# Kernel optimization log

Measured on AMD Instinct MI355X. Metric: run time of the kernel, lower is better.

The kernel has to match this reference:

```python
import jax, jax.numpy as jnp
import numpy as np
from jax import lax

B, TENC, TBERT, TOUT = 16, 168, 96, 200
NMEL, ENC, ARNN, DRNN, PRE, ATT, NF, K = 80, 512, 1024, 1024, 256, 128, 32, 31
PAD = (K - 1) // 2


def setup_inputs():
    key = jax.random.key(0)
    ks = iter(jax.random.split(key, 40))
    def rn(shape, s=0.05):
        return jax.random.normal(next(ks), shape, dtype=jnp.float32) * s
    return dict(
        memory=rn((B, TENC, ENC), 1.0),
        embeddings=rn((B, TBERT, ENC), 1.0),
        decoder_inputs=rn((B, NMEL, TOUT), 1.0),
        prenet_w1=rn((PRE, NMEL)), prenet_w2=rn((PRE, PRE)),
        prenetb_w1=rn((PRE, NMEL)), prenetb_w2=rn((PRE, PRE)),
        arnn_wih=rn((4 * ARNN, PRE + ENC)), arnn_whh=rn((4 * ARNN, ARNN)), arnn_b=rn((4 * ARNN,)),
        arnnb_wih=rn((4 * ARNN, PRE + ENC)), arnnb_whh=rn((4 * ARNN, ARNN)), arnnb_b=rn((4 * ARNN,)),
        attn_q=rn((ATT, ARNN)), attn_m=rn((ATT, ENC)), attn_conv=rn((NF, 2, K)),
        attn_loc=rn((ATT, NF)), attn_v=rn((ATT,)),
        attnb_q=rn((ATT, ARNN)), attnb_m=rn((ATT, ENC)), attnb_conv=rn((NF, 2, K)),
        attnb_loc=rn((ATT, NF)), attnb_v=rn((ATT,)),
        drnn_wih=rn((4 * DRNN, 2 * ARNN + 2 * ENC)), drnn_whh=rn((4 * DRNN, DRNN)), drnn_b=rn((4 * DRNN,)),
        drnnb_wih=rn((4 * DRNN, ARNN + ENC)), drnnb_whh=rn((4 * DRNN, DRNN)), drnnb_b=rn((4 * DRNN,)),
        proj_w=rn((NMEL, DRNN + 2 * ENC)), proj_b=rn((NMEL,)),
        gate_w=rn((1, DRNN + 2 * ENC)), gate_b=rn((1,)),
    )


def _lstm(x, h, c, wih, whh, b):
    g = x @ wih.T + h @ whh.T + b
    i, f, gg, o = jnp.split(g, 4, axis=-1)
    c = jax.nn.sigmoid(f) * c + jax.nn.sigmoid(i) * jnp.tanh(gg)
    h = jax.nn.sigmoid(o) * jnp.tanh(c)
    return h, c


def _lsa(query, mem, pmem, aw, awc, qW, convW, locW, v):
    # location-sensitive attention (Tacotron2)
    pq = query @ qW.T                                   # [B, ATT]
    cat = jnp.stack([aw, awc], axis=1)                  # [B, 2, T]
    fmap = lax.conv_general_dilated(cat, convW, (1,), [(PAD, PAD)],
                                    dimension_numbers=('NCH', 'OIH', 'NCH'))  # [B, NF, T]
    ploc = jnp.einsum('bft,af->bta', fmap, locW)        # [B, T, ATT]
    e = jnp.einsum('a,bta->bt', v, jnp.tanh(pq[:, None, :] + ploc + pmem))
    w = jax.nn.softmax(e, axis=-1)
    ctx = jnp.einsum('bt,bte->be', w, mem)
    return ctx, w


def _forward(memory, embeddings, decoder_inputs, prenet_w1, prenet_w2, prenetb_w1, prenetb_w2,
             arnn_wih, arnn_whh, arnn_b, arnnb_wih, arnnb_whh, arnnb_b,
             attn_q, attn_m, attn_conv, attn_loc, attn_v,
             attnb_q, attnb_m, attnb_conv, attnb_loc, attnb_v,
             drnn_wih, drnn_whh, drnn_b, drnnb_wih, drnnb_whh, drnnb_b,
             proj_w, proj_b, gate_w, gate_b):
    Bv, Tenc, enc = memory.shape
    Tbert = embeddings.shape[1]
    nmel = decoder_inputs.shape[1]
    arnn = arnn_whh.shape[1]
    drnn = drnn_whh.shape[1]
    pmem = jnp.einsum('bte,ae->bta', memory, attn_m)
    pbert = jnp.einsum('bte,ae->bta', embeddings, attnb_m)
    frames = jnp.moveaxis(decoder_inputs, 2, 0)         # [T, B, nmel]
    go = jnp.zeros((1, Bv, nmel), decoder_inputs.dtype)
    xs = jnp.concatenate([go, frames[:-1]], axis=0)     # teacher forcing (shifted)
    z = lambda d: jnp.zeros((Bv, d), memory.dtype)
    carry0 = (z(arnn), z(arnn), z(arnn), z(arnn), z(drnn), z(drnn), z(drnn), z(drnn),
              jnp.zeros((Bv, Tenc), memory.dtype), jnp.zeros((Bv, Tenc), memory.dtype),
              jnp.zeros((Bv, Tbert), memory.dtype), jnp.zeros((Bv, Tbert), memory.dtype),
              z(enc), z(enc))

    def step(carry, x):
        ah, ac, ahb, acb, dh, dc, dhb, dcb, aw, awc, awb, awcb, ctx, ctxb = carry
        p = jax.nn.relu(jax.nn.relu(x @ prenet_w1.T) @ prenet_w2.T)
        pb = jax.nn.relu(jax.nn.relu(x @ prenetb_w1.T) @ prenetb_w2.T)
        ah, ac = _lstm(jnp.concatenate([p, ctx], -1), ah, ac, arnn_wih, arnn_whh, arnn_b)
        ahb, acb = _lstm(jnp.concatenate([pb, ctxb], -1), ahb, acb, arnnb_wih, arnnb_whh, arnnb_b)
        ctx, aw = _lsa(ah, memory, pmem, aw, awc, attn_q, attn_conv, attn_loc, attn_v)
        awc = awc + aw
        ctxb, awb = _lsa(ahb, embeddings, pbert, awb, awcb, attnb_q, attnb_conv, attnb_loc, attnb_v)
        awcb = awcb + awb
        dh, dc = _lstm(jnp.concatenate([ah, ahb, ctx, ctxb], -1), dh, dc, drnn_wih, drnn_whh, drnn_b)
        dhb, dcb = _lstm(jnp.concatenate([ahb, ctxb], -1), dhb, dcb, drnnb_wih, drnnb_whh, drnnb_b)
        hcat = jnp.concatenate([dh, ctx, ctxb], -1)
        mel = hcat @ proj_w.T + proj_b
        gate = (hcat @ gate_w.T + gate_b)[:, 0]
        new_carry = (ah, ac, ahb, acb, dh, dc, dhb, dcb, aw, awc, awb, awcb, ctx, ctxb)
        return new_carry, (mel, gate, aw, awb)

    _, (mels, gates, aligns, alignsb) = lax.scan(step, carry0, xs)
    mel_out = jnp.transpose(mels, (1, 2, 0))            # [B, nmel, T]
    gate_out = jnp.transpose(gates, (1, 0))             # [B, T]
    align_out = jnp.transpose(aligns, (1, 0, 2))        # [B, T, Tenc]
    alignb_out = jnp.transpose(alignsb, (1, 0, 2))      # [B, T, Tbert]
    return mel_out, gate_out, align_out, alignb_out


def reference(memory, embeddings, decoder_inputs, prenet_w1, prenet_w2, prenetb_w1, prenetb_w2,
              arnn_wih, arnn_whh, arnn_b, arnnb_wih, arnnb_whh, arnnb_b,
              attn_q, attn_m, attn_conv, attn_loc, attn_v,
              attnb_q, attnb_m, attnb_conv, attnb_loc, attnb_v,
              drnn_wih, drnn_whh, drnn_b, drnnb_wih, drnnb_whh, drnnb_b,
              proj_w, proj_b, gate_w, gate_b):
    return _forward(memory, embeddings, decoder_inputs, prenet_w1, prenet_w2, prenetb_w1, prenetb_w2,
                    arnn_wih, arnn_whh, arnn_b, arnnb_wih, arnnb_whh, arnnb_b,
                    attn_q, attn_m, attn_conv, attn_loc, attn_v,
                    attnb_q, attnb_m, attnb_conv, attnb_loc, attnb_v,
                    drnn_wih, drnn_whh, drnn_b, drnnb_wih, drnnb_whh, drnnb_b,
                    proj_w, proj_b, gate_w, gate_b)
```

## Files before the change

kernel.cpp:

```cpp
#include <hip/hip_runtime.h>
#include <cstdint>
#include <cmath>

#define DEVI __device__ __forceinline__

constexpr int B_ = 16, TENC_ = 168, TBERT_ = 96, TOUT_ = 200;
constexpr int NMEL_ = 80, ENC_ = 512, ARNN_ = 1024, PRE_ = 256, ATT_ = 128, NF_ = 32, KCV_ = 31;

constexpr size_t o_qWTa = 0;
constexpr size_t o_qWTb = o_qWTa + 1024*128;
constexpr size_t o_pall  = o_qWTb + 1024*128;
constexpr size_t o_pball = o_pall + (size_t)TOUT_*B_*PRE_;
constexpr size_t o_pmem  = o_pball + (size_t)TOUT_*B_*PRE_;
constexpr size_t o_pbert = o_pmem + (size_t)B_*TENC_*ATT_;
constexpr size_t o_state = o_pbert + (size_t)B_*TBERT_*ATT_;
constexpr size_t o_ah   = o_state;
constexpr size_t o_ahb  = o_ah  + 2*B_*ARNN_;
constexpr size_t o_ac   = o_ahb + 2*B_*ARNN_;
constexpr size_t o_acb  = o_ac  + B_*ARNN_;
constexpr size_t o_dh   = o_acb + B_*ARNN_;
constexpr size_t o_dc   = o_dh  + B_*ARNN_;
constexpr size_t o_dhb  = o_dc  + B_*ARNN_;
constexpr size_t o_dcb  = o_dhb + B_*ARNN_;
constexpr size_t o_ctx  = o_dcb + B_*ARNN_;
constexpr size_t o_ctxb = o_ctx + B_*ENC_;
constexpr size_t o_aw   = o_ctxb+ B_*ENC_;
constexpr size_t o_awc  = o_aw  + B_*TENC_;
constexpr size_t o_awb  = o_awc + B_*TENC_;
constexpr size_t o_awcb = o_awb + B_*TBERT_;
constexpr size_t o_zend = o_awcb+ B_*TBERT_;
constexpr size_t ZCOUNT = o_zend - o_state;
constexpr size_t o_gd   = o_zend;
constexpr size_t o_gdb  = o_gd + 4096*B_;
constexpr size_t o_dhall   = o_gdb + 4096*B_;
constexpr size_t o_ctxall  = o_dhall + (size_t)TOUT_*B_*ARNN_;
constexpr size_t o_ctxball = o_ctxall + (size_t)TOUT_*B_*ENC_;

constexpr size_t OO_MEL  = 0;
constexpr size_t OO_GATE = (size_t)B_*NMEL_*TOUT_;
constexpr size_t OO_AL   = OO_GATE + (size_t)B_*TOUT_;
constexpr size_t OO_ALB  = OO_AL + (size_t)B_*TOUT_*TENC_;

DEVI float sigf(float x) { return 1.f / (1.f + expf(-x)); }

DEVI float dotseg(const float* __restrict__ w, const float* __restrict__ x, int n) {
  const float4* wp = reinterpret_cast<const float4*>(w);
  const float4* xp = reinterpret_cast<const float4*>(x);
  float a0 = 0, a1 = 0, a2 = 0, a3 = 0;
  int n4 = n >> 2;
#pragma unroll 4
  for (int i = 0; i < n4; ++i) {
    float4 wv = wp[i], xv = xp[i];
    a0 = fmaf(wv.x, xv.x, a0); a1 = fmaf(wv.y, xv.y, a1);
    a2 = fmaf(wv.z, xv.z, a2); a3 = fmaf(wv.w, xv.w, a3);
  }
  return (a0 + a1) + (a2 + a3);
}

__global__ __launch_bounds__(256) void k_prolog(
    const float* __restrict__ dec, const float* __restrict__ pw1, const float* __restrict__ pw2,
    const float* __restrict__ pbw1, const float* __restrict__ pbw2,
    const float* __restrict__ memory, const float* __restrict__ embeddings,
    const float* __restrict__ am, const float* __restrict__ abm,
    const float* __restrict__ aq, const float* __restrict__ abq,
    float* __restrict__ ws)
{
  __shared__ float smem[10240];
  int bid = blockIdx.x, tid = threadIdx.x;
  if (bid < 200) {
    int t = bid;
    float* xl  = smem;
    float* h1  = smem + 1280;
    float* h1b = smem + 1280 + 4096;
    for (int i = tid; i < 16*80; i += 256) {
      int b = i / 80, m = i % 80;
      xl[i] = (t == 0) ? 0.f : dec[((size_t)b*80 + m)*200 + (t-1)];
    }
    __syncthreads();
    int j = tid;
    for (int b = 0; b < 16; ++b) {
      const float* x = xl + b*80;
      float a1 = 0, a2 = 0;
#pragma unroll 4
      for (int m = 0; m < 80; ++m) { a1 = fmaf(pw1[j*80+m], x[m], a1); a2 = fmaf(pbw1[j*80+m], x[m], a2); }
      h1[b*256+j]  = fmaxf(a1, 0.f);
      h1b[b*256+j] = fmaxf(a2, 0.f);
    }
    __syncthreads();
    for (int b = 0; b < 16; ++b) {
      float a1 = 0, a2 = 0;
#pragma unroll 4
      for (int k = 0; k < 256; ++k) { a1 = fmaf(pw2[j*256+k], h1[b*256+k], a1); a2 = fmaf(pbw2[j*256+k], h1b[b*256+k], a2); }
      ws[o_pall  + ((size_t)t*16+b)*256 + j] = fmaxf(a1, 0.f);
      ws[o_pball + ((size_t)t*16+b)*256 + j] = fmaxf(a2, 0.f);
    }
  } else if (bid < 368) {
    int r0 = (bid - 200) * 16;
    float* ml = smem;
    for (int i = tid; i < 16*512; i += 256) ml[i] = memory[(size_t)r0*512 + i];
    __syncthreads();
    int a = tid & 127, ro = tid >> 7;
    for (int row = ro; row < 16; row += 2) {
      const float* x = ml + row*512; const float* w = am + (size_t)a*512;
      float acc = 0;
#pragma unroll 4
      for (int e = 0; e < 512; ++e) acc = fmaf(w[e], x[e], acc);
      ws[o_pmem + (size_t)(r0+row)*128 + a] = acc;
    }
  } else if (bid < 464) {
    int r0 = (bid - 368) * 16;
    float* ml = smem;
    for (int i = tid; i < 16*512; i += 256) ml[i] = embeddings[(size_t)r0*512 + i];
    __syncthreads();
    int a = tid & 127, ro = tid >> 7;
    for (int row = ro; row < 16; row += 2) {
      const float* x = ml + row*512; const float* w = abm + (size_t)a*512;
      float acc = 0;
#pragma unroll 4
      for (int e = 0; e < 512; ++e) acc = fmaf(w[e], x[e], acc);
      ws[o_pbert + (size_t)(r0+row)*128 + a] = acc;
    }
  } else if (bid < 466) {
    const float* src = (bid == 464) ? aq : abq;
    float* dst = ws + ((bid == 464) ? o_qWTa : o_qWTb);
    for (int i = tid; i < 1024*128; i += 256) {
      int k = i >> 7, a = i & 127;
      dst[i] = src[(size_t)a*1024 + k];
    }
  } else {
    int zi = bid - 466;
    for (size_t i = (size_t)zi*256 + tid; i < ZCOUNT; i += 8*256) ws[o_state + i] = 0.f;
  }
}


DEVI void compute_group(const float4* __restrict__ xsf, int g, int lane,
                        const float4 w[8], float acc[8][16]) {
#pragma unroll
  for (int b = 0; b < 16; ++b) {
    float4 xv = xsf[b*130 + g*64 + lane];
#pragma unroll
    for (int r = 0; r < 8; ++r) {
      acc[r][b] = fmaf(w[r].x, xv.x, acc[r][b]);
      acc[r][b] = fmaf(w[r].y, xv.y, acc[r][b]);
      acc[r][b] = fmaf(w[r].z, xv.z, acc[r][b]);
      acc[r][b] = fmaf(w[r].w, xv.w, acc[r][b]);
    }
  }
}

template<int IH>
DEVI void lstm_gates(const float* __restrict__ Wih, const float* __restrict__ Whh,
                     const float* const pieces[4], const int plens[4], int np,
                     const float* __restrict__ hp,
                     int u0, int wvi, int lane, int tid, float* __restrict__ smem,
                     float acc[8][16])
{
#pragma unroll 1
  for (int sub = 0; sub < 2; ++sub) {
    const float* W = sub ? Whh : Wih;
    const int len = sub ? 1024 : IH;
#pragma unroll 1
    for (int c0 = 0; c0 < len; c0 += 512) {
      const int n = (len - c0 < 512) ? (len - c0) : 512;
      __syncthreads();
      if (sub == 0) {
#pragma unroll 1
        for (int b = 0; b < 16; ++b)
          for (int k = tid; k < n; k += 256) {
            int off = c0 + k;
            const float* src = pieces[0]; int L = plens[0];
            if (np > 1 && off >= L) {
              off -= L; src = pieces[1]; L = plens[1];
              if (np > 2 && off >= L) {
                off -= L; src = pieces[2]; L = plens[2];
                if (np > 3 && off >= L) { off -= L; src = pieces[3]; L = plens[3]; }
              }
            }
            smem[b*520 + k] = src[(size_t)b*L + off];
          }
      } else {
#pragma unroll 1
        for (int b = 0; b < 16; ++b)
          for (int k = tid; k < n; k += 256)
            smem[b*520 + k] = hp[b*1024 + c0 + k];
      }
      __syncthreads();
      const int ng = n >> 8;
      const float* wbase = W + (size_t)(wvi*1024 + u0)*len + c0 + 4*lane;
      const float4* xsf = (const float4*)smem;
      float4 w0[8], w1[8];
#pragma unroll
      for (int r = 0; r < 8; ++r) w0[r] = *(const float4*)(wbase + (size_t)r*len);
      if (ng == 2) {
#pragma unroll
        for (int r = 0; r < 8; ++r) w1[r] = *(const float4*)(wbase + (size_t)r*len + 256);
        compute_group(xsf, 0, lane, w0, acc);
        compute_group(xsf, 1, lane, w1, acc);
      } else {
        compute_group(xsf, 0, lane, w0, acc);
      }
    }
  }
}

DEVI void wave_reduce(float acc[8][16], float* __restrict__ red, int lane, float res[4]) {
  int o = lane & 31, half = lane >> 5;
#pragma unroll
  for (int ph = 0; ph < 4; ++ph) {
#pragma unroll
    for (int j = 0; j < 32; ++j)
      red[j*68 + lane] = acc[2*ph + (j >> 4)][j & 15];
    float s = 0;
    const float* rrow = red + o*68 + half*32;
#pragma unroll
    for (int j = 0; j < 8; ++j) {
      float4 v = *(const float4*)(rrow + 4*j);
      s += (v.x + v.y) + (v.z + v.w);
    }
    res[ph] = s + __shfl_xor(s, 32);
  }
}

__global__ __launch_bounds__(256, 2) void k_step1(
    int t,
    const float* __restrict__ a_wih, const float* __restrict__ a_whh, const float* __restrict__ a_b,
    const float* __restrict__ ab_wih, const float* __restrict__ ab_whh, const float* __restrict__ ab_b,
    const float* __restrict__ d_wih, const float* __restrict__ d_whh,
    const float* __restrict__ db_wih, const float* __restrict__ db_whh,
    float* __restrict__ ws)
{
  __shared__ __align__(16) float smem[8704];
  __shared__ float gbuf[512];
  int bid = blockIdx.x, tid = threadIdx.x;
  int wvi = tid >> 6, lane = tid & 63;
  int type = bid >> 7, idx = bid & 127, u0 = idx * 8;

  float acc[8][16];
#pragma unroll
  for (int r = 0; r < 8; ++r)
#pragma unroll
    for (int b = 0; b < 16; ++b) acc[r][b] = 0.f;

  float res[4];
  int o = lane & 31;

  if (type <= 1) {
    if (t >= TOUT_) return;
    bool isB = (type == 1);
    const float* pieces[4] = { ws + (isB ? o_pball : o_pall) + (size_t)t*B_*PRE_,
                               ws + (isB ? o_ctxb : o_ctx), nullptr, nullptr };
    const int plens[4] = { 256, 512, 0, 0 };
    const float* hp = ws + (isB ? o_ahb : o_ah) + (size_t)((t+1)&1)*(B_*ARNN_);
    lstm_gates<768>(isB ? ab_wih : a_wih, isB ? ab_whh : a_whh, pieces, plens, 2, hp,
                    u0, wvi, lane, tid, smem, acc);
    __syncthreads();
    wave_reduce(acc, smem + wvi*(32*68), lane, res);
    const float* bias = isB ? ab_b : a_b;
#pragma unroll
    for (int ph = 0; ph < 4; ++ph) {
      if (lane < 32) {
        int j = 2*ph + (o >> 4), b = o & 15;
        gbuf[wvi*128 + j*16 + b] = res[ph] + bias[wvi*1024 + u0 + j];
      }
    }
    __syncthreads();
    if (tid < 128) {
      int j = tid >> 4, b = tid & 15, u = u0 + j;
      float gi = gbuf[0*128 + j*16 + b], gf = gbuf[1*128 + j*16 + b];
      float gg = gbuf[2*128 + j*16 + b], go = gbuf[3*128 + j*16 + b];
      float* cst  = ws + (isB ? o_acb : o_ac);
      float* hcur = ws + (isB ? o_ahb : o_ah) + (size_t)(t&1)*(B_*ARNN_);
      float co = cst[u*16 + b];
      float cn = sigf(gf)*co + sigf(gi)*tanhf(gg);
      float hn = sigf(go)*tanhf(cn);
      cst[u*16 + b] = cn;
      hcur[b*1024 + u] = hn;
    }
  } else if (type == 2) {
    if (t == 0) return;
    const float* pieces[4] = { ws + o_ah  + (size_t)((t-1)&1)*(B_*ARNN_),
                               ws + o_ahb + (size_t)((t-1)&1)*(B_*ARNN_),
                               ws + o_ctx, ws + o_ctxb };
    const int plens[4] = { 1024, 1024, 512, 512 };
    lstm_gates<3072>(d_wih, d_whh, pieces, plens, 4, ws + o_dh,
                     u0, wvi, lane, tid, smem, acc);
    __syncthreads();
    wave_reduce(acc, smem + wvi*(32*68), lane, res);
    float* gout = ws + o_gd;
#pragma unroll
    for (int ph = 0; ph < 4; ++ph)
      if (lane < 32)
        gout[(size_t)(wvi*1024 + u0 + 2*ph + (o >> 4))*16 + (o & 15)] = res[ph];
  } else {
    if (t == 0) return;
    const float* pieces[4] = { ws + o_ahb + (size_t)((t-1)&1)*(B_*ARNN_),
                               ws + o_ctxb, nullptr, nullptr };
    const int plens[4] = { 1024, 512, 0, 0 };
    lstm_gates<1536>(db_wih, db_whh, pieces, plens, 2, ws + o_dhb,
                     u0, wvi, lane, tid, smem, acc);
    __syncthreads();
    wave_reduce(acc, smem + wvi*(32*68), lane, res);
    float* gout = ws + o_gdb;
#pragma unroll
    for (int ph = 0; ph < 4; ++ph)
      if (lane < 32)
        gout[(size_t)(wvi*1024 + u0 + 2*ph + (o >> 4))*16 + (o & 15)] = res[ph];
  }
}

__global__ __launch_bounds__(512) void k_step2(
    int t, const float* __restrict__ memory, const float* __restrict__ embeddings,
    const float* __restrict__ a_conv, const float* __restrict__ a_loc, const float* __restrict__ a_v,
    const float* __restrict__ ab_conv, const float* __restrict__ ab_loc, const float* __restrict__ ab_v,
    const float* __restrict__ d_b, const float* __restrict__ db_b,
    float* __restrict__ ws, float* __restrict__ out)
{
  __shared__ float ah_l[1024];
  __shared__ float pqp[4][128];
  __shared__ float pq_s[128];
  __shared__ float awp[2][TENC_+32];
  __shared__ float cw_s[NF_*2*KCV_];
  __shared__ float vv[128];
  __shared__ float fmT[TENC_][NF_];
  __shared__ float ep[TENC_][2];
  __shared__ float wl[TENC_];
  __shared__ float smx[2];
  int bid = blockIdx.x, tid = threadIdx.x;

  if (bid < 32) {
    if (t >= TOUT_) return;
    bool isB = bid >= 16; int b = bid & 15;
    int T = isB ? TBERT_ : TENC_;
    const float* mem   = isB ? embeddings : memory;
    const float* pmemB = ws + (isB ? o_pbert : o_pmem);
    const float* qWT   = ws + (isB ? o_qWTb : o_qWTa);
    const float* convW = isB ? ab_conv : a_conv;
    const float* locW  = isB ? ab_loc : a_loc;
    const float* vW    = isB ? ab_v : a_v;
    const float* hq = ws + (isB ? o_ahb : o_ah) + (size_t)(t&1)*(B_*ARNN_) + b*ARNN_;
    float* awS  = ws + (isB ? o_awb : o_aw) + b*T;
    float* awcS = ws + (isB ? o_awcb : o_awc) + b*T;
    float* ctxS = ws + (isB ? o_ctxb : o_ctx) + b*ENC_;
    float* ctxAll = ws + (isB ? o_ctxball : o_ctxall) + ((size_t)t*16 + b)*ENC_;
    float* alOut = out + (isB ? OO_ALB : OO_AL) + ((size_t)b*TOUT_ + t)*T;

    for (int i = tid; i < 1024; i += 512) ah_l[i] = hq[i];
    for (int i = tid; i < NF_*2*KCV_; i += 512) cw_s[i] = convW[i];
    for (int i = tid; i < 128; i += 512) vv[i] = vW[i];
    for (int i = tid; i < T + 30; i += 512) {
      bool in = (i >= 15) && (i < T + 15);
      awp[0][i] = in ? awS[i-15] : 0.f;
      awp[1][i] = in ? awcS[i-15] : 0.f;
    }
    __syncthreads();
    {
      int a = tid & 127, hf = tid >> 7;
      float acc = 0;
      for (int k = hf*256; k < hf*256 + 256; ++k) acc = fmaf(qWT[(size_t)k*128 + a], ah_l[k], acc);
      pqp[hf][a] = acc;
    }
    __syncthreads();
    if (tid < 128) pq_s[tid] = pqp[0][tid] + pqp[1][tid] + pqp[2][tid] + pqp[3][tid];
    __syncthreads();
    for (int idx = tid; idx < T*NF_; idx += 512) {
      int tt = idx >> 5, f = idx & 31;
      const float* c0 = cw_s + f*62;
      float s = 0;
#pragma unroll
      for (int kk = 0; kk < 31; ++kk)
        s = fmaf(awp[0][tt+kk], c0[kk], fmaf(awp[1][tt+kk], c0[31+kk], s));
      fmT[tt][f] = s;
    }
    __syncthreads();
    {
      int a = tid & 127;
      float la[32];
#pragma unroll
      for (int f = 0; f < 32; ++f) la[f] = locW[a*32 + f];
      float pqr = pq_s[a], vr = vv[a];
      for (int idx = tid; idx < T*128; idx += 512) {
        int tt = idx >> 7;
        float pl = 0;
#pragma unroll
        for (int f = 0; f < 32; ++f) pl = fmaf(fmT[tt][f], la[f], pl);
        float s = vr * tanhf(pqr + pl + pmemB[((size_t)b*T + tt)*128 + a]);
#pragma unroll
        for (int off = 1; off < 64; off <<= 1) s += __shfl_xor(s, off);
        if ((tid & 63) == 0) ep[tt][(idx >> 6) & 1] = s;
      }
    }
    __syncthreads();
    if (tid < 64) {
      float m = -1e30f;
      for (int i = tid; i < T; i += 64) m = fmaxf(m, ep[i][0] + ep[i][1]);
#pragma unroll
      for (int off = 1; off < 64; off <<= 1) m = fmaxf(m, __shfl_xor(m, off));
      float ssum = 0;
      for (int i = tid; i < T; i += 64) ssum += expf(ep[i][0] + ep[i][1] - m);
#pragma unroll
      for (int off = 1; off < 64; off <<= 1) ssum += __shfl_xor(ssum, off);
      if (tid == 0) { smx[0] = m; smx[1] = 1.f / ssum; }
    }
    __syncthreads();
    for (int i = tid; i < T; i += 512) {
      float wv = expf(ep[i][0] + ep[i][1] - smx[0]) * smx[1];
      wl[i] = wv;
      awS[i] = wv;
      awcS[i] += wv;
      alOut[i] = wv;
    }
    __syncthreads();
    {
      float a0 = 0, a1 = 0, a2 = 0, a3 = 0;
      const float* mb = mem + (size_t)b*T*512 + tid;
      int tt = 0;
      for (; tt + 4 <= T; tt += 4) {
        a0 = fmaf(wl[tt],   mb[(size_t)tt*512],     a0);
        a1 = fmaf(wl[tt+1], mb[(size_t)(tt+1)*512], a1);
        a2 = fmaf(wl[tt+2], mb[(size_t)(tt+2)*512], a2);
        a3 = fmaf(wl[tt+3], mb[(size_t)(tt+3)*512], a3);
      }
      for (; tt < T; ++tt) a0 = fmaf(wl[tt], mb[(size_t)tt*512], a0);
      float acc = (a0 + a1) + (a2 + a3);
      ctxS[tid] = acc;
      ctxAll[tid] = acc;
    }
  } else {
    if (t == 0) return;
    int gid = (bid - 32)*512 + tid;
#pragma unroll
    for (int r = 0; r < 2; ++r) {
      int uf = gid + r*16384;
      int L = uf >> 14;
      int rem = uf & 16383;
      int u = rem >> 4, b = rem & 15;
      const float* g = ws + (L ? o_gdb : o_gd);
      const float* bias = L ? db_b : d_b;
      float* h  = ws + (L ? o_dhb : o_dh);
      float* cc = ws + (L ? o_dcb : o_dc);
      float gi = g[(size_t)u*16 + b]        + bias[u];
      float gf = g[(size_t)(1024+u)*16 + b] + bias[1024+u];
      float gg = g[(size_t)(2048+u)*16 + b] + bias[2048+u];
      float go = g[(size_t)(3072+u)*16 + b] + bias[3072+u];
      float co = cc[u*16 + b];
      float cn = sigf(gf)*co + sigf(gi)*tanhf(gg);
      float hn = sigf(go)*tanhf(cn);
      cc[u*16 + b] = cn;
      h[b*1024 + u] = hn;
      if (L == 0) ws[o_dhall + ((size_t)(t-1)*16 + b)*1024 + u] = hn;
    }
  }
}

__global__ __launch_bounds__(512) void k_proj(
    const float* __restrict__ pw, const float* __restrict__ pb,
    const float* __restrict__ gw, const float* __restrict__ gb,
    const float* __restrict__ ws, float* __restrict__ out)
{
  int t = blockIdx.x, tid = threadIdx.x;
  for (int o = tid; o < 16*81; o += 512) {
    int b = o / 81, j = o % 81;
    const float* wrow = (j < 80) ? (pw + (size_t)j*2048) : gw;
    const float* xd  = ws + o_dhall   + ((size_t)t*16 + b)*1024;
    const float* xc  = ws + o_ctxall  + ((size_t)t*16 + b)*512;
    const float* xcb = ws + o_ctxball + ((size_t)t*16 + b)*512;
    float acc = dotseg(wrow, xd, 1024) + dotseg(wrow + 1024, xc, 512)
              + dotseg(wrow + 1536, xcb, 512) + ((j < 80) ? pb[j] : gb[0]);
    if (j < 80) out[OO_MEL + ((size_t)b*80 + j)*200 + t] = acc;
    else        out[OO_GATE + (size_t)b*200 + t] = acc;
  }
}

extern "C" void kernel_launch(void* const* d_in, const int* in_sizes, int n_in,
                              void* d_out, int out_size, void* d_ws, size_t ws_size,
                              hipStream_t stream) {
  (void)in_sizes; (void)n_in; (void)out_size; (void)ws_size;
  const float* memory   = (const float*)d_in[0];
  const float* embeddings = (const float*)d_in[1];
  const float* dec      = (const float*)d_in[2];
  const float* pw1      = (const float*)d_in[3];
  const float* pw2      = (const float*)d_in[4];
  const float* pbw1     = (const float*)d_in[5];
  const float* pbw2     = (const float*)d_in[6];
  const float* a_wih    = (const float*)d_in[7];
  const float* a_whh    = (const float*)d_in[8];
  const float* a_b      = (const float*)d_in[9];
  const float* ab_wih   = (const float*)d_in[10];
  const float* ab_whh   = (const float*)d_in[11];
  const float* ab_b     = (const float*)d_in[12];
  const float* a_q      = (const float*)d_in[13];
  const float* a_m      = (const float*)d_in[14];
  const float* a_conv   = (const float*)d_in[15];
  const float* a_loc    = (const float*)d_in[16];
  const float* a_v      = (const float*)d_in[17];
  const float* ab_q     = (const float*)d_in[18];
  const float* ab_m     = (const float*)d_in[19];
  const float* ab_conv  = (const float*)d_in[20];
  const float* ab_loc   = (const float*)d_in[21];
  const float* ab_v     = (const float*)d_in[22];
  const float* d_wih    = (const float*)d_in[23];
  const float* d_whh    = (const float*)d_in[24];
  const float* d_b      = (const float*)d_in[25];
  const float* db_wih   = (const float*)d_in[26];
  const float* db_whh   = (const float*)d_in[27];
  const float* db_b     = (const float*)d_in[28];
  const float* proj_w   = (const float*)d_in[29];
  const float* proj_b   = (const float*)d_in[30];
  const float* gate_w   = (const float*)d_in[31];
  const float* gate_b   = (const float*)d_in[32];
  float* ws  = (float*)d_ws;
  float* out = (float*)d_out;

  k_prolog<<<dim3(474), dim3(256), 0, stream>>>(dec, pw1, pw2, pbw1, pbw2,
      memory, embeddings, a_m, ab_m, a_q, ab_q, ws);
  for (int t = 0; t <= TOUT_; ++t) {
    k_step1<<<dim3(512), dim3(256), 0, stream>>>(t,
        a_wih, a_whh, a_b, ab_wih, ab_whh, ab_b, d_wih, d_whh, db_wih, db_whh, ws);
    k_step2<<<dim3(64), dim3(512), 0, stream>>>(t, memory, embeddings,
        a_conv, a_loc, a_v, ab_conv, ab_loc, ab_v, d_b, db_b, ws, out);
  }
  k_proj<<<dim3(200), dim3(512), 0, stream>>>(proj_w, proj_b, gate_w, gate_b, ws, out);
}
```

Baseline: 34.28 ms.

## Fuse per-step kernels into a persistent cooperative kernel with grid syncs

```diff
diff --git a/kernel.cpp b/kernel.cpp
--- a/kernel.cpp
+++ b/kernel.cpp
@@ -1,6 +1,9 @@
 #include <hip/hip_runtime.h>
+#include <hip/hip_cooperative_groups.h>
 #include <cstdint>
 #include <cmath>
+
+namespace cg = cooperative_groups;
 
 #define DEVI __device__ __forceinline__
 
@@ -57,6 +60,12 @@
   return (a0 + a1) + (a2 + a3);
 }
 
+DEVI void gl_lds16(const float* g, float* l) {
+  auto gp = (const __attribute__((address_space(1))) float*)g;
+  auto lp = (__attribute__((address_space(3))) float*)l;
+  __builtin_amdgcn_global_load_lds(gp, lp, 16, 0, 0);
+}
+
 __global__ __launch_bounds__(256) void k_prolog(
     const float* __restrict__ dec, const float* __restrict__ pw1, const float* __restrict__ pw2,
     const float* __restrict__ pbw1, const float* __restrict__ pbw2,
@@ -133,73 +142,59 @@
   }
 }
 
-
-DEVI void compute_group(const float4* __restrict__ xsf, int g, int lane,
-                        const float4 w[8], float acc[8][16]) {
+DEVI const float* seg_src(int type, int k0, int b, int t, const float* __restrict__ ws) {
+  if (type <= 1) {
+    if (k0 < 256)  return ws + (type ? o_pball : o_pall) + ((size_t)t*16 + b)*256 + k0;
+    if (k0 < 768)  return ws + (type ? o_ctxb : o_ctx) + (size_t)b*512 + (k0 - 256);
+    return ws + (type ? o_ahb : o_ah) + (size_t)((t+1)&1)*(B_*ARNN_) + (size_t)b*1024 + (k0 - 768);
+  } else if (type == 2) {
+    int tp = (t-1) & 1;
+    if (k0 < 1024) return ws + o_ah  + (size_t)tp*(B_*ARNN_) + (size_t)b*1024 + k0;
+    if (k0 < 2048) return ws + o_ahb + (size_t)tp*(B_*ARNN_) + (size_t)b*1024 + (k0-1024);
+    if (k0 < 2560) return ws + o_ctx  + (size_t)b*512 + (k0-2048);
+    if (k0 < 3072) return ws + o_ctxb + (size_t)b*512 + (k0-2560);
+    return ws + o_dh + (size_t)b*1024 + (k0-3072);
+  } else {
+    int tp = (t-1) & 1;
+    if (k0 < 1024) return ws + o_ahb + (size_t)tp*(B_*ARNN_) + (size_t)b*1024 + k0;
+    if (k0 < 1536) return ws + o_ctxb + (size_t)b*512 + (k0-1024);
+    return ws + o_dhb + (size_t)b*1024 + (k0-1536);
+  }
+}
+
+DEVI void fillr(int type, int r, float* __restrict__ dst, int wl, int lane, int t,
+                const float* __restrict__ ws) {
+  int k0 = r * 256;
+#pragma unroll
+  for (int o = 0; o < 4; ++o) {
+    int b = o*4 + wl;
+    const float* s = seg_src(type, k0, b, t, ws) + 4*lane;
+    gl_lds16(s, dst + b*256);
+  }
+}
+
+DEVI void loadw(float4 w[8], const float* __restrict__ Wih, const float* __restrict__ Whh,
+                int IH, int row0, int r, int lane) {
+  int k0 = r * 256;
+  const float* base; size_t st;
+  if (k0 < IH) { base = Wih + (size_t)row0*IH + k0; st = IH; }
+  else         { base = Whh + (size_t)row0*1024 + (k0 - IH); st = 1024; }
+  base += 4*lane;
+#pragma unroll
+  for (int i = 0; i < 8; ++i) w[i] = *(const float4*)(base + st*i);
+}
+
+DEVI void computeg(const float* __restrict__ buf, const float4 w[8], int lane, float acc[8][16]) {
+  const float4* xb = (const float4*)buf;
 #pragma unroll
   for (int b = 0; b < 16; ++b) {
-    float4 xv = xsf[b*130 + g*64 + lane];
-#pragma unroll
-    for (int r = 0; r < 8; ++r) {
-      acc[r][b] = fmaf(w[r].x, xv.x, acc[r][b]);
-      acc[r][b] = fmaf(w[r].y, xv.y, acc[r][b]);
-      acc[r][b] = fmaf(w[r].z, xv.z, acc[r][b]);
-      acc[r][b] = fmaf(w[r].w, xv.w, acc[r][b]);
-    }
-  }
-}
-
-template<int IH>
-DEVI void lstm_gates(const float* __restrict__ Wih, const float* __restrict__ Whh,
-                     const float* const pieces[4], const int plens[4], int np,
-                     const float* __restrict__ hp,
-                     int u0, int wvi, int lane, int tid, float* __restrict__ smem,
-                     float acc[8][16])
-{
-#pragma unroll 1
-  for (int sub = 0; sub < 2; ++sub) {
-    const float* W = sub ? Whh : Wih;
-    const int len = sub ? 1024 : IH;
-#pragma unroll 1
-    for (int c0 = 0; c0 < len; c0 += 512) {
-      const int n = (len - c0 < 512) ? (len - c0) : 512;
-      __syncthreads();
-      if (sub == 0) {
-#pragma unroll 1
-        for (int b = 0; b < 16; ++b)
-          for (int k = tid; k < n; k += 256) {
-            int off = c0 + k;
-            const float* src = pieces[0]; int L = plens[0];
-            if (np > 1 && off >= L) {
-              off -= L; src = pieces[1]; L = plens[1];
-              if (np > 2 && off >= L) {
-                off -= L; src = pieces[2]; L = plens[2];
-                if (np > 3 && off >= L) { off -= L; src = pieces[3]; L = plens[3]; }
-              }
-            }
-            smem[b*520 + k] = src[(size_t)b*L + off];
-          }
-      } else {
-#pragma unroll 1
-        for (int b = 0; b < 16; ++b)
-          for (int k = tid; k < n; k += 256)
-            smem[b*520 + k] = hp[b*1024 + c0 + k];
-      }
-      __syncthreads();
-      const int ng = n >> 8;
-      const float* wbase = W + (size_t)(wvi*1024 + u0)*len + c0 + 4*lane;
-      const float4* xsf = (const float4*)smem;
-      float4 w0[8], w1[8];
-#pragma unroll
-      for (int r = 0; r < 8; ++r) w0[r] = *(const float4*)(wbase + (size_t)r*len);
-      if (ng == 2) {
-#pragma unroll
-        for (int r = 0; r < 8; ++r) w1[r] = *(const float4*)(wbase + (size_t)r*len + 256);
-        compute_group(xsf, 0, lane, w0, acc);
-        compute_group(xsf, 1, lane, w1, acc);
-      } else {
-        compute_group(xsf, 0, lane, w0, acc);
-      }
+    float4 xv = xb[b*64 + lane];
+#pragma unroll
+    for (int rr = 0; rr < 8; ++rr) {
+      acc[rr][b] = fmaf(w[rr].x, xv.x, acc[rr][b]);
+      acc[rr][b] = fmaf(w[rr].y, xv.y, acc[rr][b]);
+      acc[rr][b] = fmaf(w[rr].z, xv.z, acc[rr][b]);
+      acc[rr][b] = fmaf(w[rr].w, xv.w, acc[rr][b]);
     }
   }
 }
@@ -222,234 +217,235 @@
   }
 }
 
-__global__ __launch_bounds__(256, 2) void k_step1(
-    int t,
+__global__ __launch_bounds__(512, 2) void k_persist(
+    const float* __restrict__ memory, const float* __restrict__ embeddings,
     const float* __restrict__ a_wih, const float* __restrict__ a_whh, const float* __restrict__ a_b,
     const float* __restrict__ ab_wih, const float* __restrict__ ab_whh, const float* __restrict__ ab_b,
-    const float* __restrict__ d_wih, const float* __restrict__ d_whh,
-    const float* __restrict__ db_wih, const float* __restrict__ db_whh,
-    float* __restrict__ ws)
+    const float* __restrict__ d_wih, const float* __restrict__ d_whh, const float* __restrict__ d_b,
+    const float* __restrict__ db_wih, const float* __restrict__ db_whh, const float* __restrict__ db_b,
+    const float* __restrict__ a_conv, const float* __restrict__ a_loc, const float* __restrict__ a_v,
+    const float* __restrict__ ab_conv, const float* __restrict__ ab_loc, const float* __restrict__ ab_v,
+    float* __restrict__ ws, float* __restrict__ out)
 {
-  __shared__ __align__(16) float smem[8704];
-  __shared__ float gbuf[512];
+  __shared__ __align__(16) float dlds[16384];
+  cg::grid_group grid = cg::this_grid();
   int bid = blockIdx.x, tid = threadIdx.x;
-  int wvi = tid >> 6, lane = tid & 63;
-  int type = bid >> 7, idx = bid & 127, u0 = idx * 8;
-
-  float acc[8][16];
-#pragma unroll
-  for (int r = 0; r < 8; ++r)
-#pragma unroll
-    for (int b = 0; b < 16; ++b) acc[r][b] = 0.f;
-
-  float res[4];
-  int o = lane & 31;
-
-  if (type <= 1) {
-    if (t >= TOUT_) return;
-    bool isB = (type == 1);
-    const float* pieces[4] = { ws + (isB ? o_pball : o_pall) + (size_t)t*B_*PRE_,
-                               ws + (isB ? o_ctxb : o_ctx), nullptr, nullptr };
-    const int plens[4] = { 256, 512, 0, 0 };
-    const float* hp = ws + (isB ? o_ahb : o_ah) + (size_t)((t+1)&1)*(B_*ARNN_);
-    lstm_gates<768>(isB ? ab_wih : a_wih, isB ? ab_whh : a_whh, pieces, plens, 2, hp,
-                    u0, wvi, lane, tid, smem, acc);
-    __syncthreads();
-    wave_reduce(acc, smem + wvi*(32*68), lane, res);
-    const float* bias = isB ? ab_b : a_b;
-#pragma unroll
-    for (int ph = 0; ph < 4; ++ph) {
-      if (lane < 32) {
+  int wv = tid >> 6, lane = tid & 63;
+  int half = wv >> 2, wl = wv & 3;
+  int grp = bid >> 7, oct = bid & 127, u0 = oct * 8;
+  int type = (half == 0) ? grp : 2 + grp;
+
+  int R, IH; const float *Wih, *Whh;
+  switch (type) {
+    case 0:  R = 7;  IH = 768;  Wih = a_wih;  Whh = a_whh;  break;
+    case 1:  R = 7;  IH = 768;  Wih = ab_wih; Whh = ab_whh; break;
+    case 2:  R = 16; IH = 3072; Wih = d_wih;  Whh = d_whh;  break;
+    default: R = 10; IH = 1536; Wih = db_wih; Whh = db_whh; break;
+  }
+  int row0 = wl*1024 + u0;
+  float* mybuf = dlds + half*8192;
+
+  for (int t = 0; t <= TOUT_; ++t) {
+    bool act = (type <= 1) ? (t < TOUT_) : (t >= 1);
+    int R0 = (t < TOUT_) ? 7 : 0;
+    int R1 = (t >= 1) ? (grp ? 10 : 16) : 0;
+    int maxr = (R0 > R1) ? R0 : R1;
+
+    float acc[8][16];
+#pragma unroll
+    for (int rr = 0; rr < 8; ++rr)
+#pragma unroll
+      for (int b = 0; b < 16; ++b) acc[rr][b] = 0.f;
+
+    float4 wc[8];
+    if (act) { fillr(type, 0, mybuf, wl, lane, t, ws); loadw(wc, Wih, Whh, IH, row0, 0, lane); }
+    __syncthreads();
+    int p = 0;
+    for (int r = 0; r < maxr; ++r) {
+      float4 wn[8];
+      bool a0 = act && (r < R);
+      bool a1 = act && (r + 1 < R);
+      if (a1) { fillr(type, r+1, mybuf + (p^1)*4096, wl, lane, t, ws);
+                loadw(wn, Wih, Whh, IH, row0, r+1, lane); }
+      if (a0) computeg(mybuf + p*4096, wc, lane, acc);
+      __syncthreads();
+      p ^= 1;
+#pragma unroll
+      for (int i = 0; i < 8; ++i) wc[i] = wn[i];
+    }
+
+    float res[4];
+    if (half == 0 && act) wave_reduce(acc, dlds + wl*2176, lane, res);
+    __syncthreads();
+    if (half == 1 && act) wave_reduce(acc, dlds + wl*2176, lane, res);
+    if (half == 1 && act && lane < 32) {
+      float* gout = ws + (grp ? o_gdb : o_gd);
+      int o = lane;
+#pragma unroll
+      for (int ph = 0; ph < 4; ++ph)
+        gout[(size_t)(wl*1024 + u0 + 2*ph + (o >> 4))*16 + (o & 15)] = res[ph];
+    }
+    __syncthreads();
+    if (half == 0 && act && lane < 32) {
+      const float* bias = grp ? ab_b : a_b;
+      int o = lane;
+#pragma unroll
+      for (int ph = 0; ph < 4; ++ph) {
         int j = 2*ph + (o >> 4), b = o & 15;
-        gbuf[wvi*128 + j*16 + b] = res[ph] + bias[wvi*1024 + u0 + j];
+        dlds[wl*128 + j*16 + b] = res[ph] + bias[wl*1024 + u0 + j];
       }
     }
     __syncthreads();
-    if (tid < 128) {
+    if (tid < 128 && t < TOUT_) {
       int j = tid >> 4, b = tid & 15, u = u0 + j;
-      float gi = gbuf[0*128 + j*16 + b], gf = gbuf[1*128 + j*16 + b];
-      float gg = gbuf[2*128 + j*16 + b], go = gbuf[3*128 + j*16 + b];
-      float* cst  = ws + (isB ? o_acb : o_ac);
-      float* hcur = ws + (isB ? o_ahb : o_ah) + (size_t)(t&1)*(B_*ARNN_);
+      float gi = dlds[0*128 + j*16+b], gf = dlds[1*128 + j*16+b];
+      float gg = dlds[2*128 + j*16+b], go = dlds[3*128 + j*16+b];
+      float* cst  = ws + (grp ? o_acb : o_ac);
+      float* hcur = ws + (grp ? o_ahb : o_ah) + (size_t)(t&1)*(B_*ARNN_);
       float co = cst[u*16 + b];
       float cn = sigf(gf)*co + sigf(gi)*tanhf(gg);
       float hn = sigf(go)*tanhf(cn);
       cst[u*16 + b] = cn;
       hcur[b*1024 + u] = hn;
     }
-  } else if (type == 2) {
-    if (t == 0) return;
-    const float* pieces[4] = { ws + o_ah  + (size_t)((t-1)&1)*(B_*ARNN_),
-                               ws + o_ahb + (size_t)((t-1)&1)*(B_*ARNN_),
-                               ws + o_ctx, ws + o_ctxb };
-    const int plens[4] = { 1024, 1024, 512, 512 };
-    lstm_gates<3072>(d_wih, d_whh, pieces, plens, 4, ws + o_dh,
-                     u0, wvi, lane, tid, smem, acc);
-    __syncthreads();
-    wave_reduce(acc, smem + wvi*(32*68), lane, res);
-    float* gout = ws + o_gd;
-#pragma unroll
-    for (int ph = 0; ph < 4; ++ph)
-      if (lane < 32)
-        gout[(size_t)(wvi*1024 + u0 + 2*ph + (o >> 4))*16 + (o & 15)] = res[ph];
-  } else {
-    if (t == 0) return;
-    const float* pieces[4] = { ws + o_ahb + (size_t)((t-1)&1)*(B_*ARNN_),
-                               ws + o_ctxb, nullptr, nullptr };
-    const int plens[4] = { 1024, 512, 0, 0 };
-    lstm_gates<1536>(db_wih, db_whh, pieces, plens, 2, ws + o_dhb,
-                     u0, wvi, lane, tid, smem, acc);
-    __syncthreads();
-    wave_reduce(acc, smem + wvi*(32*68), lane, res);
-    float* gout = ws + o_gdb;
-#pragma unroll
-    for (int ph = 0; ph < 4; ++ph)
-      if (lane < 32)
-        gout[(size_t)(wvi*1024 + u0 + 2*ph + (o >> 4))*16 + (o & 15)] = res[ph];
-  }
-}
-
-__global__ __launch_bounds__(512) void k_step2(
-    int t, const float* __restrict__ memory, const float* __restrict__ embeddings,
-    const float* __restrict__ a_conv, const float* __restrict__ a_loc, const float* __restrict__ a_v,
-    const float* __restrict__ ab_conv, const float* __restrict__ ab_loc, const float* __restrict__ ab_v,
-    const float* __restrict__ d_b, const float* __restrict__ db_b,
-    float* __restrict__ ws, float* __restrict__ out)
-{
-  __shared__ float ah_l[1024];
-  __shared__ float pqp[4][128];
-  __shared__ float pq_s[128];
-  __shared__ float awp[2][TENC_+32];
-  __shared__ float cw_s[NF_*2*KCV_];
-  __shared__ float vv[128];
-  __shared__ float fmT[TENC_][NF_];
-  __shared__ float ep[TENC_][2];
-  __shared__ float wl[TENC_];
-  __shared__ float smx[2];
-  int bid = blockIdx.x, tid = threadIdx.x;
-
-  if (bid < 32) {
-    if (t >= TOUT_) return;
-    bool isB = bid >= 16; int b = bid & 15;
-    int T = isB ? TBERT_ : TENC_;
-    const float* mem   = isB ? embeddings : memory;
-    const float* pmemB = ws + (isB ? o_pbert : o_pmem);
-    const float* qWT   = ws + (isB ? o_qWTb : o_qWTa);
-    const float* convW = isB ? ab_conv : a_conv;
-    const float* locW  = isB ? ab_loc : a_loc;
-    const float* vW    = isB ? ab_v : a_v;
-    const float* hq = ws + (isB ? o_ahb : o_ah) + (size_t)(t&1)*(B_*ARNN_) + b*ARNN_;
-    float* awS  = ws + (isB ? o_awb : o_aw) + b*T;
-    float* awcS = ws + (isB ? o_awcb : o_awc) + b*T;
-    float* ctxS = ws + (isB ? o_ctxb : o_ctx) + b*ENC_;
-    float* ctxAll = ws + (isB ? o_ctxball : o_ctxall) + ((size_t)t*16 + b)*ENC_;
-    float* alOut = out + (isB ? OO_ALB : OO_AL) + ((size_t)b*TOUT_ + t)*T;
-
-    for (int i = tid; i < 1024; i += 512) ah_l[i] = hq[i];
-    for (int i = tid; i < NF_*2*KCV_; i += 512) cw_s[i] = convW[i];
-    for (int i = tid; i < 128; i += 512) vv[i] = vW[i];
-    for (int i = tid; i < T + 30; i += 512) {
-      bool in = (i >= 15) && (i < T + 15);
-      awp[0][i] = in ? awS[i-15] : 0.f;
-      awp[1][i] = in ? awcS[i-15] : 0.f;
-    }
-    __syncthreads();
-    {
-      int a = tid & 127, hf = tid >> 7;
-      float acc = 0;
-      for (int k = hf*256; k < hf*256 + 256; ++k) acc = fmaf(qWT[(size_t)k*128 + a], ah_l[k], acc);
-      pqp[hf][a] = acc;
-    }
-    __syncthreads();
-    if (tid < 128) pq_s[tid] = pqp[0][tid] + pqp[1][tid] + pqp[2][tid] + pqp[3][tid];
-    __syncthreads();
-    for (int idx = tid; idx < T*NF_; idx += 512) {
-      int tt = idx >> 5, f = idx & 31;
-      const float* c0 = cw_s + f*62;
-      float s = 0;
-#pragma unroll
-      for (int kk = 0; kk < 31; ++kk)
-        s = fmaf(awp[0][tt+kk], c0[kk], fmaf(awp[1][tt+kk], c0[31+kk], s));
-      fmT[tt][f] = s;
-    }
-    __syncthreads();
-    {
-      int a = tid & 127;
-      float la[32];
-#pragma unroll
-      for (int f = 0; f < 32; ++f) la[f] = locW[a*32 + f];
-      float pqr = pq_s[a], vr = vv[a];
-      for (int idx = tid; idx < T*128; idx += 512) {
-        int tt = idx >> 7;
-        float pl = 0;
-#pragma unroll
-        for (int f = 0; f < 32; ++f) pl = fmaf(fmT[tt][f], la[f], pl);
-        float s = vr * tanhf(pqr + pl + pmemB[((size_t)b*T + tt)*128 + a]);
-#pragma unroll
-        for (int off = 1; off < 64; off <<= 1) s += __shfl_xor(s, off);
-        if ((tid & 63) == 0) ep[tt][(idx >> 6) & 1] = s;
+    grid.sync();
+
+    if (bid < 32) {
+      if (t < TOUT_) {
+        bool isB = bid >= 16; int b = bid & 15;
+        int T = isB ? TBERT_ : TENC_;
+        const float* mem   = isB ? embeddings : memory;
+        const float* pmemB = ws + (isB ? o_pbert : o_pmem);
+        const float* qWT   = ws + (isB ? o_qWTb : o_qWTa);
+        const float* convW = isB ? ab_conv : a_conv;
+        const float* locW  = isB ? ab_loc : a_loc;
+        const float* vW    = isB ? ab_v : a_v;
+        const float* hq = ws + (isB ? o_ahb : o_ah) + (size_t)(t&1)*(B_*ARNN_) + (size_t)b*ARNN_;
+        float* awS  = ws + (isB ? o_awb : o_aw) + (size_t)b*T;
+        float* awcS = ws + (isB ? o_awcb : o_awc) + (size_t)b*T;
+        float* ctxS = ws + (isB ? o_ctxb : o_ctx) + (size_t)b*ENC_;
+        float* ctxAll = ws + (isB ? o_ctxball : o_ctxall) + ((size_t)t*16 + b)*ENC_;
+        float* alOut = out + (isB ? OO_ALB : OO_AL) + ((size_t)b*TOUT_ + t)*T;
+
+        float* ah_l = dlds;
+        float* pqp  = dlds + 1024;
+        float* pq_s = dlds + 1536;
+        float* awp0 = dlds + 1664;
+        float* awp1 = dlds + 1872;
+        float* cw_s = dlds + 2080;
+        float* vv   = dlds + 4064;
+        float* fmT  = dlds + 4192;
+        float* ep_s = dlds + 9568;
+        float* wl_s = dlds + 9904;
+        float* smx  = dlds + 10072;
+
+        for (int i = tid; i < 1024; i += 512) ah_l[i] = hq[i];
+        for (int i = tid; i < NF_*2*KCV_; i += 512) cw_s[i] = convW[i];
+        for (int i = tid; i < 128; i += 512) vv[i] = vW[i];
+        for (int i = tid; i < T + 30; i += 512) {
+          bool in = (i >= 15) && (i < T + 15);
+          awp0[i] = in ? awS[i-15] : 0.f;
+          awp1[i] = in ? awcS[i-15] : 0.f;
+        }
+        __syncthreads();
+        {
+          int a = tid & 127, hf = tid >> 7;
+          float acc2 = 0;
+          for (int k = hf*256; k < hf*256 + 256; ++k) acc2 = fmaf(qWT[(size_t)k*128 + a], ah_l[k], acc2);
+          pqp[hf*128 + a] = acc2;
+        }
+        __syncthreads();
+        if (tid < 128) pq_s[tid] = pqp[tid] + pqp[128+tid] + pqp[256+tid] + pqp[384+tid];
+        __syncthreads();
+        for (int idx = tid; idx < T*NF_; idx += 512) {
+          int tt = idx >> 5, f = idx & 31;
+          const float* c0 = cw_s + f*62;
+          float s = 0;
+#pragma unroll
+          for (int kk = 0; kk < 31; ++kk)
+            s = fmaf(awp0[tt+kk], c0[kk], fmaf(awp1[tt+kk], c0[31+kk], s));
+          fmT[tt*32 + f] = s;
+        }
+        __syncthreads();
+        {
+          int a = tid & 127;
+          float la[32];
+#pragma unroll
+          for (int f = 0; f < 32; ++f) la[f] = locW[a*32 + f];
+          float pqr = pq_s[a], vr = vv[a];
+          for (int idx = tid; idx < T*128; idx += 512) {
+            int tt = idx >> 7;
+            float pl = 0;
+#pragma unroll
+            for (int f = 0; f < 32; ++f) pl = fmaf(fmT[tt*32 + f], la[f], pl);
+            float s = vr * tanhf(pqr + pl + pmemB[((size_t)b*T + tt)*128 + a]);
+#pragma unroll
+            for (int off = 1; off < 64; off <<= 1) s += __shfl_xor(s, off);
+            if ((tid & 63) == 0) ep_s[tt*2 + ((idx >> 6) & 1)] = s;
+          }
+        }
+        __syncthreads();
+        if (tid < 64) {
+          float m = -1e30f;
+          for (int i = tid; i < T; i += 64) m = fmaxf(m, ep_s[2*i] + ep_s[2*i+1]);
+#pragma unroll
+          for (int off = 1; off < 64; off <<= 1) m = fmaxf(m, __shfl_xor(m, off));
+          float ssum = 0;
+          for (int i = tid; i < T; i += 64) ssum += expf(ep_s[2*i] + ep_s[2*i+1] - m);
+#pragma unroll
+          for (int off = 1; off < 64; off <<= 1) ssum += __shfl_xor(ssum, off);
+          if (tid == 0) { smx[0] = m; smx[1] = 1.f / ssum; }
+        }
+        __syncthreads();
+        for (int i = tid; i < T; i += 512) {
+          float wv2 = expf(ep_s[2*i] + ep_s[2*i+1] - smx[0]) * smx[1];
+          wl_s[i] = wv2;
+          awS[i] = wv2;
+          awcS[i] += wv2;
+          alOut[i] = wv2;
+        }
+        __syncthreads();
+        {
+          float a0 = 0, a1 = 0, a2 = 0, a3 = 0;
+          const float* mb = mem + (size_t)b*T*512 + tid;
+          int tt = 0;
+          for (; tt + 4 <= T; tt += 4) {
+            a0 = fmaf(wl_s[tt],   mb[(size_t)tt*512],     a0);
+            a1 = fmaf(wl_s[tt+1], mb[(size_t)(tt+1)*512], a1);
+            a2 = fmaf(wl_s[tt+2], mb[(size_t)(tt+2)*512], a2);
+            a3 = fmaf(wl_s[tt+3], mb[(size_t)(tt+3)*512], a3);
+          }
+          for (; tt < T; ++tt) a0 = fmaf(wl_s[tt], mb[(size_t)tt*512], a0);
+          float acc2 = (a0 + a1) + (a2 + a3);
+          ctxS[tid] = acc2;
+          ctxAll[tid] = acc2;
+        }
       }
-    }
-    __syncthreads();
-    if (tid < 64) {
-      float m = -1e30f;
-      for (int i = tid; i < T; i += 64) m = fmaxf(m, ep[i][0] + ep[i][1]);
-#pragma unroll
-      for (int off = 1; off < 64; off <<= 1) m = fmaxf(m, __shfl_xor(m, off));
-      float ssum = 0;
-      for (int i = tid; i < T; i += 64) ssum += expf(ep[i][0] + ep[i][1] - m);
-#pragma unroll
-      for (int off = 1; off < 64; off <<= 1) ssum += __shfl_xor(ssum, off);
-      if (tid == 0) { smx[0] = m; smx[1] = 1.f / ssum; }
-    }
-    __syncthreads();
-    for (int i = tid; i < T; i += 512) {
-      float wv = expf(ep[i][0] + ep[i][1] - smx[0]) * smx[1];
-      wl[i] = wv;
-      awS[i] = wv;
-      awcS[i] += wv;
-      alOut[i] = wv;
-    }
-    __syncthreads();
-    {
-      float a0 = 0, a1 = 0, a2 = 0, a3 = 0;
-      const float* mb = mem + (size_t)b*T*512 + tid;
-      int tt = 0;
-      for (; tt + 4 <= T; tt += 4) {
-        a0 = fmaf(wl[tt],   mb[(size_t)tt*512],     a0);
-        a1 = fmaf(wl[tt+1], mb[(size_t)(tt+1)*512], a1);
-        a2 = fmaf(wl[tt+2], mb[(size_t)(tt+2)*512], a2);
-        a3 = fmaf(wl[tt+3], mb[(size_t)(tt+3)*512], a3);
+    } else {
+      if (t >= 1) {
+        int gid = (bid - 32)*512 + tid;
+        if (gid < 32768) {
+          int L = gid >> 14;
+          int rem = gid & 16383;
+          int u = rem >> 4, b = rem & 15;
+          const float* g = ws + (L ? o_gdb : o_gd);
+          const float* bias = L ? db_b : d_b;
+          float* h  = ws + (L ? o_dhb : o_dh);
+          float* cc = ws + (L ? o_dcb : o_dc);
+          float gi = g[(size_t)u*16 + b]        + bias[u];
+          float gf = g[(size_t)(1024+u)*16 + b] + bias[1024+u];
+          float gg = g[(size_t)(2048+u)*16 + b] + bias[2048+u];
+          float go = g[(size_t)(3072+u)*16 + b] + bias[3072+u];
+          float co = cc[u*16 + b];
+          float cn = sigf(gf)*co + sigf(gi)*tanhf(gg);
+          float hn = sigf(go)*tanhf(cn);
+          cc[u*16 + b] = cn;
+          h[b*1024 + u] = hn;
+          if (L == 0) ws[o_dhall + ((size_t)(t-1)*16 + b)*1024 + u] = hn;
+        }
       }
-      for (; tt < T; ++tt) a0 = fmaf(wl[tt], mb[(size_t)tt*512], a0);
-      float acc = (a0 + a1) + (a2 + a3);
-      ctxS[tid] = acc;
-      ctxAll[tid] = acc;
-    }
-  } else {
-    if (t == 0) return;
-    int gid = (bid - 32)*512 + tid;
-#pragma unroll
-    for (int r = 0; r < 2; ++r) {
-      int uf = gid + r*16384;
-      int L = uf >> 14;
-      int rem = uf & 16383;
-      int u = rem >> 4, b = rem & 15;
-      const float* g = ws + (L ? o_gdb : o_gd);
-      const float* bias = L ? db_b : d_b;
-      float* h  = ws + (L ? o_dhb : o_dh);
-      float* cc = ws + (L ? o_dcb : o_dc);
-      float gi = g[(size_t)u*16 + b]        + bias[u];
-      float gf = g[(size_t)(1024+u)*16 + b] + bias[1024+u];
-      float gg = g[(size_t)(2048+u)*16 + b] + bias[2048+u];
-      float go = g[(size_t)(3072+u)*16 + b] + bias[3072+u];
-      float co = cc[u*16 + b];
-      float cn = sigf(gf)*co + sigf(gi)*tanhf(gg);
-      float hn = sigf(go)*tanhf(cn);
-      cc[u*16 + b] = cn;
-      h[b*1024 + u] = hn;
-      if (L == 0) ws[o_dhall + ((size_t)(t-1)*16 + b)*1024 + u] = hn;
-    }
+    }
+    grid.sync();
   }
 }
 
@@ -476,7 +472,7 @@
                               void* d_out, int out_size, void* d_ws, size_t ws_size,
                               hipStream_t stream) {
   (void)in_sizes; (void)n_in; (void)out_size; (void)ws_size;
-  const float* memory   = (const float*)d_in[0];
+  const float* memory     = (const float*)d_in[0];
   const float* embeddings = (const float*)d_in[1];
   const float* dec      = (const float*)d_in[2];
   const float* pw1      = (const float*)d_in[3];
@@ -514,11 +510,19 @@
 
   k_prolog<<<dim3(474), dim3(256), 0, stream>>>(dec, pw1, pw2, pbw1, pbw2,
       memory, embeddings, a_m, ab_m, a_q, ab_q, ws);
-  for (int t = 0; t <= TOUT_; ++t) {
-    k_step1<<<dim3(512), dim3(256), 0, stream>>>(t,
-        a_wih, a_whh, a_b, ab_wih, ab_whh, ab_b, d_wih, d_whh, db_wih, db_whh, ws);
-    k_step2<<<dim3(64), dim3(512), 0, stream>>>(t, memory, embeddings,
-        a_conv, a_loc, a_v, ab_conv, ab_loc, ab_v, d_b, db_b, ws, out);
-  }
+
+  void* args[] = {
+    (void*)&memory, (void*)&embeddings,
+    (void*)&a_wih, (void*)&a_whh, (void*)&a_b,
+    (void*)&ab_wih, (void*)&ab_whh, (void*)&ab_b,
+    (void*)&d_wih, (void*)&d_whh, (void*)&d_b,
+    (void*)&db_wih, (void*)&db_whh, (void*)&db_b,
+    (void*)&a_conv, (void*)&a_loc, (void*)&a_v,
+    (void*)&ab_conv, (void*)&ab_loc, (void*)&ab_v,
+    (void*)&ws, (void*)&out
+  };
+  hipLaunchCooperativeKernel(reinterpret_cast<void*>(&k_persist),
+                             dim3(256), dim3(512), args, 0, stream);
+
   k_proj<<<dim3(200), dim3(512), 0, stream>>>(proj_w, proj_b, gate_w, gate_b, ws, out);
 }
```

After: 43.93 ms. +28.2%, slower.
